# Kernel optimization log

Measured on AMD Instinct MI355X. Metric: run time of the kernel, lower is better.

The kernel has to match this reference:

```python
import jax, jax.numpy as jnp
import numpy as np

N_NODES = 100000
N_EDGES = 3200000
IN_C, HID_C, OUT_C = 128, 16, 5
NEG_SLOPE = 0.2


def setup_inputs() -> dict:
    key = jax.random.key(0)
    ks = jax.random.split(key, 12)
    x = jax.random.normal(ks[0], (N_NODES, IN_C), dtype=jnp.float32)
    edge_index = jax.random.randint(ks[1], (2, N_EDGES), 0, N_NODES, dtype=jnp.int64)
    # GATConv layer 1 params (heads=1)
    s1 = 1.0 / np.sqrt(IN_C)
    W1 = jax.random.uniform(ks[2], (IN_C, HID_C), jnp.float32, -s1, s1)
    att_src1 = jax.random.uniform(ks[3], (HID_C,), jnp.float32, -1.0, 1.0) * s1
    att_dst1 = jax.random.uniform(ks[4], (HID_C,), jnp.float32, -1.0, 1.0) * s1
    b1 = jnp.zeros((HID_C,), jnp.float32)
    # GATConv layer 2 params
    s2 = 1.0 / np.sqrt(HID_C)
    W2 = jax.random.uniform(ks[5], (HID_C, OUT_C), jnp.float32, -s2, s2)
    att_src2 = jax.random.uniform(ks[6], (OUT_C,), jnp.float32, -1.0, 1.0) * s2
    att_dst2 = jax.random.uniform(ks[7], (OUT_C,), jnp.float32, -1.0, 1.0) * s2
    b2 = jnp.zeros((OUT_C,), jnp.float32)
    return {"x": x, "edge_index": edge_index,
            "W1": W1, "att_src1": att_src1, "att_dst1": att_dst1, "b1": b1,
            "W2": W2, "att_src2": att_src2, "att_dst2": att_dst2, "b2": b2}


def gat_layer(x, src, dst, W, att_src, att_dst, bias, n_nodes):
    # project: [N, C_out]
    h = x @ W
    a_src = h @ att_src  # [N]
    a_dst = h @ att_dst  # [N]
    e = a_src[src] + a_dst[dst]            # [E]
    e = jax.nn.leaky_relu(e, NEG_SLOPE)
    # per-destination-node softmax over incoming edges (stable)
    m = jax.ops.segment_max(e, dst, num_segments=n_nodes)
    ex = jnp.exp(e - m[dst])
    denom = jax.ops.segment_sum(ex, dst, num_segments=n_nodes)
    alpha = ex / (denom[dst] + 1e-16)      # [E]
    # weighted scatter-aggregate of source features
    out = jax.ops.segment_sum(h[src] * alpha[:, None], dst, num_segments=n_nodes)
    return out + bias


def reference(x, edge_index, W1, att_src1, att_dst1, b1, W2, att_src2, att_dst2, b2):
    n = x.shape[0]
    loops = jnp.arange(n, dtype=edge_index.dtype)
    src = jnp.concatenate([edge_index[0], loops])  # add_self_loops=True
    dst = jnp.concatenate([edge_index[1], loops])
    h = gat_layer(x, src, dst, W1, att_src1, att_dst1, b1, n)
    h = jax.nn.relu(h)
    h = gat_layer(h, src, dst, W2, att_src2, att_dst2, b2, n)
    return jax.nn.log_softmax(h, axis=1)
```

## Files before the change

### kernel.cpp

```cpp
#include <hip/hip_runtime.h>

#define N_NODES 100000
#define N_EDGES 3200000
#define E_TOT   (N_EDGES + N_NODES)
#define IN_C 128
#define HID  16
#define OUTC 5
#define NEG_SLOPE 0.2f

#define NBKT 391
#define CAP  9216
#define P1_TILE 8192
#define P1_GRID ((E_TOT + P1_TILE - 1) / P1_TILE)

__global__ void zero_gcnt_k(int* __restrict__ gcnt) {
    int i = blockIdx.x * blockDim.x + threadIdx.x;
    if (i < NBKT) gcnt[i] = 0;
}

__global__ __launch_bounds__(256) void part_k(const int* __restrict__ ei,
                                              int* __restrict__ gcnt,
                                              unsigned* __restrict__ pairs) {
    __shared__ unsigned vbuf[P1_TILE];
    __shared__ unsigned short bbuf[P1_TILE];
    __shared__ int hist[NBKT];
    __shared__ int cur[NBKT];
    int t = threadIdx.x;
    for (int i = t; i < NBKT; i += 256) hist[i] = 0;
    __syncthreads();
    int base = blockIdx.x * P1_TILE;
    int lim = E_TOT - base; if (lim > P1_TILE) lim = P1_TILE;
    for (int i = t; i < lim; i += 256) {
        int e = base + i;
        int s, d;
        if (e < N_EDGES) { s = ei[e]; d = ei[N_EDGES + e]; }
        else             { s = e - N_EDGES; d = s; }
        int b = d >> 8;
        vbuf[i] = ((unsigned)s << 8) | (unsigned)(d & 255);
        bbuf[i] = (unsigned short)b;
        atomicAdd(&hist[b], 1);
    }
    __syncthreads();
    for (int i = t; i < NBKT; i += 256) {
        int h = hist[i];
        cur[i] = h ? atomicAdd(&gcnt[i], h) : 0;
    }
    __syncthreads();
    for (int i = t; i < lim; i += 256) {
        int b = bbuf[i];
        int p = atomicAdd(&cur[b], 1);
        if (p >= 0 && p < CAP) pairs[(size_t)b * CAP + p] = vbuf[i];
    }
}

__global__ void scan_gcnt_k(const int* __restrict__ gcnt, int* __restrict__ cbase) {
    __shared__ int s[512];
    int t = threadIdx.x;
    int v = (t < NBKT) ? gcnt[t] : 0;
    s[t] = v; __syncthreads();
    for (int off = 1; off < 512; off <<= 1) {
        int x = (t >= off) ? s[t - off] : 0;
        __syncthreads();
        s[t] += x;
        __syncthreads();
    }
    if (t < NBKT) cbase[t] = s[t] - v;
}

__global__ __launch_bounds__(256) void build_k(const unsigned* __restrict__ pairs,
                                               const int* __restrict__ gcnt,
                                               const int* __restrict__ cbase,
                                               int* __restrict__ csr,
                                               int* __restrict__ row_start,
                                               int* __restrict__ cnt) {
    __shared__ int c[256], s[256], cur[256];
    int t = threadIdx.x;
    int b = blockIdx.x;
    c[t] = 0;
    __syncthreads();
    int tot = gcnt[b];
    if (tot > CAP) tot = CAP;
    size_t pbase = (size_t)b * CAP;
    for (int i = t; i < tot; i += 256) atomicAdd(&c[pairs[pbase + i] & 255u], 1);
    __syncthreads();
    int v0 = c[t];
    s[t] = v0; __syncthreads();
    for (int off = 1; off < 256; off <<= 1) {
        int x = (t >= off) ? s[t - off] : 0;
        __syncthreads();
        s[t] += x;
        __syncthreads();
    }
    int excl = s[t] - v0;
    int gbase = cbase[b];
    int node = (b << 8) + t;
    if (node < N_NODES) { row_start[node] = gbase + excl; cnt[node] = v0; }
    cur[t] = gbase + excl;
    __syncthreads();
    for (int i = t; i < tot; i += 256) {
        unsigned v = pairs[pbase + i];
        int pos = atomicAdd(&cur[v & 255u], 1);
        csr[pos] = (int)(v >> 8);
    }
}

__global__ void proj1_k(const float* __restrict__ x, const float* __restrict__ W1,
                        const float* __restrict__ att_s, const float* __restrict__ att_d,
                        float* __restrict__ h1, float* __restrict__ a_src,
                        float* __restrict__ a_dst) {
    __shared__ float sW[IN_C * HID];
    __shared__ float sX[16 * IN_C];
    __shared__ float sH[16 * HID];
    int t = threadIdx.x;
    for (int i = t; i < IN_C * HID; i += 256) sW[i] = W1[i];
    int node0 = blockIdx.x * 16;
    for (int i = t; i < 16 * IN_C; i += 256) {
        int r = i >> 7, c = i & 127;
        int node = node0 + r;
        sX[i] = (node < N_NODES) ? x[(size_t)node * IN_C + c] : 0.0f;
    }
    __syncthreads();
    int r = t >> 4, c = t & 15;
    int node = node0 + r;
    float acc = 0.0f;
    #pragma unroll 8
    for (int k = 0; k < IN_C; ++k) acc += sX[r * IN_C + k] * sW[k * HID + c];
    sH[r * HID + c] = acc;
    if (node < N_NODES) h1[(size_t)node * HID + c] = acc;
    __syncthreads();
    if (c == 0 && node < N_NODES) {
        float s = 0.0f, d = 0.0f;
        #pragma unroll
        for (int k = 0; k < HID; ++k) {
            float hv = sH[r * HID + k];
            s += hv * att_s[k];
            d += hv * att_d[k];
        }
        a_src[node] = s;
        a_dst[node] = d;
    }
}

#define H2_STRIDE 8
__global__ __launch_bounds__(256) void gat1_k(
    const int* __restrict__ csr, const int* __restrict__ row_start,
    const int* __restrict__ cnt, const float* __restrict__ h1,
    const float* __restrict__ a_src1, const float* __restrict__ a_dst1,
    const float* __restrict__ b1, const float* __restrict__ W2,
    const float* __restrict__ as2, const float* __restrict__ ad2,
    float* __restrict__ h2p, float* __restrict__ a_dst2) {
    __shared__ float sW2[HID * OUTC];
    __shared__ float sB1[HID];
    __shared__ float sAs[OUTC], sAd[OUTC];
    int t = threadIdx.x;
    if (t < HID * OUTC) sW2[t] = W2[t];
    if (t < HID) sB1[t] = b1[t];
    if (t < OUTC) { sAs[t] = as2[t]; sAd[t] = ad2[t]; }
    __syncthreads();

    int node = (blockIdx.x * 256 + t) >> 4;
    int lane = t & 15;
    int start = row_start[node];
    int len   = cnt[node];
    float ad  = a_dst1[node];

    float acc[HID];
    #pragma unroll
    for (int c = 0; c < HID; ++c) acc[c] = 0.0f;
    float accd = 0.0f;
    for (int it = lane; it < len; it += 16) {
        int s = csr[start + it];
        float v = a_src1[s] + ad;
        v = (v > 0.0f) ? v : NEG_SLOPE * v;
        float ex = __expf(v);
        accd += ex;
        const float4* h4 = (const float4*)(h1 + (size_t)s * HID);
        #pragma unroll
        for (int q = 0; q < 4; ++q) {
            float4 hv = h4[q];
            acc[q * 4 + 0] += ex * hv.x;
            acc[q * 4 + 1] += ex * hv.y;
            acc[q * 4 + 2] += ex * hv.z;
            acc[q * 4 + 3] += ex * hv.w;
        }
    }
    #pragma unroll
    for (int off = 8; off; off >>= 1) {
        accd += __shfl_xor(accd, off);
        #pragma unroll
        for (int c = 0; c < HID; ++c) acc[c] += __shfl_xor(acc[c], off);
    }
    float inv = 1.0f / (accd + 1e-16f);
    float g[HID];
    #pragma unroll
    for (int k = 0; k < HID; ++k) g[k] = fmaxf(acc[k] * inv + sB1[k], 0.0f);
    float h2[OUTC];
    #pragma unroll
    for (int c = 0; c < OUTC; ++c) {
        float a = 0.0f;
        #pragma unroll
        for (int k = 0; k < HID; ++k) a += g[k] * sW2[k * OUTC + c];
        h2[c] = a;
    }
    if (lane == 0) {
        float s2 = 0.0f, d2 = 0.0f;
        #pragma unroll
        for (int c = 0; c < OUTC; ++c) { s2 += h2[c] * sAs[c]; d2 += h2[c] * sAd[c]; }
        h2p[(size_t)node * H2_STRIDE] = s2;
        a_dst2[node] = d2;
    }
    if (lane >= 1 && lane <= OUTC) {
        float hv = 0.0f;
        #pragma unroll
        for (int c = 0; c < OUTC; ++c) if (lane - 1 == c) hv = h2[c];
        h2p[(size_t)node * H2_STRIDE + lane] = hv;
    }
}

__global__ __launch_bounds__(256) void gat2_k(
    const int* __restrict__ csr, const int* __restrict__ row_start,
    const int* __restrict__ cnt, const float* __restrict__ h2p,
    const float* __restrict__ a_dst2, const float* __restrict__ b2,
    float* __restrict__ out) {
    __shared__ float sB2[OUTC];
    int t = threadIdx.x;
    if (t < OUTC) sB2[t] = b2[t];
    __syncthreads();

    int node = (blockIdx.x * 256 + t) >> 4;
    int lane = t & 15;
    int start = row_start[node];
    int len   = cnt[node];
    float ad  = a_dst2[node];

    float acc[OUTC];
    #pragma unroll
    for (int c = 0; c < OUTC; ++c) acc[c] = 0.0f;
    float accd = 0.0f;
    for (int it = lane; it < len; it += 16) {
        int s = csr[start + it];
        const float4* hp = (const float4*)(h2p + (size_t)s * H2_STRIDE);
        float4 p0 = hp[0];
        float4 p1 = hp[1];
        float v = p0.x + ad;
        v = (v > 0.0f) ? v : NEG_SLOPE * v;
        float ex = __expf(v);
        accd += ex;
        acc[0] += ex * p0.y; acc[1] += ex * p0.z; acc[2] += ex * p0.w;
        acc[3] += ex * p1.x; acc[4] += ex * p1.y;
    }
    #pragma unroll
    for (int off = 8; off; off >>= 1) {
        accd += __shfl_xor(accd, off);
        #pragma unroll
        for (int c = 0; c < OUTC; ++c) acc[c] += __shfl_xor(acc[c], off);
    }
    float inv = 1.0f / (accd + 1e-16f);
    float val[OUTC];
    float mx = -3.4e38f;
    #pragma unroll
    for (int c = 0; c < OUTC; ++c) {
        val[c] = acc[c] * inv + sB2[c];
        mx = fmaxf(mx, val[c]);
    }
    float se = 0.0f;
    #pragma unroll
    for (int c = 0; c < OUTC; ++c) se += __expf(val[c] - mx);
    float lse = logf(se) + mx;
    if (lane < OUTC) {
        float v = 0.0f;
        #pragma unroll
        for (int c = 0; c < OUTC; ++c) if (lane == c) v = val[c];
        out[(size_t)node * OUTC + lane] = v - lse;
    }
}

extern "C" void kernel_launch(void* const* d_in, const int* in_sizes, int n_in,
                              void* d_out, int out_size, void* d_ws, size_t ws_size,
                              hipStream_t stream) {
    const float* x    = (const float*)d_in[0];
    const int*   ei   = (const int*)d_in[1];
    const float* W1   = (const float*)d_in[2];
    const float* as1  = (const float*)d_in[3];
    const float* ad1  = (const float*)d_in[4];
    const float* b1   = (const float*)d_in[5];
    const float* W2   = (const float*)d_in[6];
    const float* as2  = (const float*)d_in[7];
    const float* ad2  = (const float*)d_in[8];
    const float* b2   = (const float*)d_in[9];
    float* out = (float*)d_out;

    int* wsi = (int*)d_ws;
    unsigned* pairs  = (unsigned*)wsi;
    float* h1    = (float*)wsi;
    float* h2p   = h1 + (size_t)16 * N_NODES;
    float* asrc1 = h1 + (size_t)24 * N_NODES;
    float* adst1 = h1 + (size_t)25 * N_NODES;
    float* adst2 = h1 + (size_t)26 * N_NODES;
    int* csr       = wsi + (size_t)NBKT * CAP;
    int* cnt       = csr + E_TOT;
    int* row_start = cnt + N_NODES;
    int* gcnt      = row_start + N_NODES;
    int* cbase     = gcnt + NBKT;

    const int B = 256;
    const int gW = (N_NODES * 16) / B;

    zero_gcnt_k<<<(NBKT + B - 1) / B, B, 0, stream>>>(gcnt);
    part_k<<<P1_GRID, B, 0, stream>>>(ei, gcnt, pairs);
    scan_gcnt_k<<<1, 512, 0, stream>>>(gcnt, cbase);
    build_k<<<NBKT, B, 0, stream>>>(pairs, gcnt, cbase, csr, row_start, cnt);

    proj1_k<<<(N_NODES + 15) / 16, 256, 0, stream>>>(x, W1, as1, ad1, h1, asrc1, adst1);
    gat1_k<<<gW, B, 0, stream>>>(csr, row_start, cnt, h1, asrc1, adst1, b1,
                                 W2, as2, ad2, h2p, adst2);
    gat2_k<<<gW, B, 0, stream>>>(csr, row_start, cnt, h2p, adst2, b2, out);
}
```

Baseline: 286.7 us.

## Aggregate directly from bucketed edge pairs with LDS atomics; drop CSR build; fp16 features

Removes the scan and CSR build kernels. The two GAT aggregation kernels now read the per-bucket edge pairs directly, with each 512-thread block handling half of a 256-node bucket and accumulating weighted features into shared memory through atomics. Node features h1 and h2 are stored as fp16 to cut gather bandwidth. The cost is heavy shared-memory atomic contention, each pair being read twice with half the threads skipping, and reduced precision in the features.

```diff
diff --git a/kernel.cpp b/kernel.cpp
--- a/kernel.cpp
+++ b/kernel.cpp
@@ -1,4 +1,5 @@
 #include <hip/hip_runtime.h>
+#include <hip/hip_fp16.h>
 
 #define N_NODES 100000
 #define N_EDGES 3200000
@@ -12,6 +13,14 @@
 #define CAP  9216
 #define P1_TILE 8192
 #define P1_GRID ((E_TOT + P1_TILE - 1) / P1_TILE)
+
+__device__ __forceinline__ float pk_half2(float a, float b) {
+    __half2 h = __halves2half2(__float2half(a), __float2half(b));
+    return *(float*)&h;
+}
+__device__ __forceinline__ float2 unpk_half2(float v) {
+    return __half22float2(*(__half2*)&v);
+}
 
 __global__ void zero_gcnt_k(int* __restrict__ gcnt) {
     int i = blockIdx.x * blockDim.x + threadIdx.x;
@@ -53,60 +62,9 @@
     }
 }
 
-__global__ void scan_gcnt_k(const int* __restrict__ gcnt, int* __restrict__ cbase) {
-    __shared__ int s[512];
-    int t = threadIdx.x;
-    int v = (t < NBKT) ? gcnt[t] : 0;
-    s[t] = v; __syncthreads();
-    for (int off = 1; off < 512; off <<= 1) {
-        int x = (t >= off) ? s[t - off] : 0;
-        __syncthreads();
-        s[t] += x;
-        __syncthreads();
-    }
-    if (t < NBKT) cbase[t] = s[t] - v;
-}
-
-__global__ __launch_bounds__(256) void build_k(const unsigned* __restrict__ pairs,
-                                               const int* __restrict__ gcnt,
-                                               const int* __restrict__ cbase,
-                                               int* __restrict__ csr,
-                                               int* __restrict__ row_start,
-                                               int* __restrict__ cnt) {
-    __shared__ int c[256], s[256], cur[256];
-    int t = threadIdx.x;
-    int b = blockIdx.x;
-    c[t] = 0;
-    __syncthreads();
-    int tot = gcnt[b];
-    if (tot > CAP) tot = CAP;
-    size_t pbase = (size_t)b * CAP;
-    for (int i = t; i < tot; i += 256) atomicAdd(&c[pairs[pbase + i] & 255u], 1);
-    __syncthreads();
-    int v0 = c[t];
-    s[t] = v0; __syncthreads();
-    for (int off = 1; off < 256; off <<= 1) {
-        int x = (t >= off) ? s[t - off] : 0;
-        __syncthreads();
-        s[t] += x;
-        __syncthreads();
-    }
-    int excl = s[t] - v0;
-    int gbase = cbase[b];
-    int node = (b << 8) + t;
-    if (node < N_NODES) { row_start[node] = gbase + excl; cnt[node] = v0; }
-    cur[t] = gbase + excl;
-    __syncthreads();
-    for (int i = t; i < tot; i += 256) {
-        unsigned v = pairs[pbase + i];
-        int pos = atomicAdd(&cur[v & 255u], 1);
-        csr[pos] = (int)(v >> 8);
-    }
-}
-
 __global__ void proj1_k(const float* __restrict__ x, const float* __restrict__ W1,
                         const float* __restrict__ att_s, const float* __restrict__ att_d,
-                        float* __restrict__ h1, float* __restrict__ a_src,
+                        __half* __restrict__ h1f, float* __restrict__ a_src,
                         float* __restrict__ a_dst) {
     __shared__ float sW[IN_C * HID];
     __shared__ float sX[16 * IN_C];
@@ -126,7 +84,7 @@
     #pragma unroll 8
     for (int k = 0; k < IN_C; ++k) acc += sX[r * IN_C + k] * sW[k * HID + c];
     sH[r * HID + c] = acc;
-    if (node < N_NODES) h1[(size_t)node * HID + c] = acc;
+    if (node < N_NODES) h1f[(size_t)node * HID + c] = __float2half(acc);
     __syncthreads();
     if (c == 0 && node < N_NODES) {
         float s = 0.0f, d = 0.0f;
@@ -141,137 +99,144 @@
     }
 }
 
-#define H2_STRIDE 8
-__global__ __launch_bounds__(256) void gat1_k(
-    const int* __restrict__ csr, const int* __restrict__ row_start,
-    const int* __restrict__ cnt, const float* __restrict__ h1,
-    const float* __restrict__ a_src1, const float* __restrict__ a_dst1,
-    const float* __restrict__ b1, const float* __restrict__ W2,
-    const float* __restrict__ as2, const float* __restrict__ ad2,
-    float* __restrict__ h2p, float* __restrict__ a_dst2) {
+__global__ __launch_bounds__(512) void gat1b_k(
+    const unsigned* __restrict__ pairs, const int* __restrict__ gcnt,
+    const __half* __restrict__ h1f, const float* __restrict__ asrc1,
+    const float* __restrict__ adst1, const float* __restrict__ b1,
+    const float* __restrict__ W2, const float* __restrict__ as2,
+    const float* __restrict__ ad2, float4* __restrict__ h2p,
+    float* __restrict__ adst2) {
+    __shared__ float acc[128][17];
+    __shared__ float adt[128];
     __shared__ float sW2[HID * OUTC];
     __shared__ float sB1[HID];
     __shared__ float sAs[OUTC], sAd[OUTC];
     int t = threadIdx.x;
+    int bk = blockIdx.x >> 1, hh = blockIdx.x & 1;
+    for (int i = t; i < 128 * 17; i += 512) ((float*)acc)[i] = 0.0f;
     if (t < HID * OUTC) sW2[t] = W2[t];
-    if (t < HID) sB1[t] = b1[t];
-    if (t < OUTC) { sAs[t] = as2[t]; sAd[t] = ad2[t]; }
-    __syncthreads();
-
-    int node = (blockIdx.x * 256 + t) >> 4;
-    int lane = t & 15;
-    int start = row_start[node];
-    int len   = cnt[node];
-    float ad  = a_dst1[node];
-
-    float acc[HID];
-    #pragma unroll
-    for (int c = 0; c < HID; ++c) acc[c] = 0.0f;
-    float accd = 0.0f;
-    for (int it = lane; it < len; it += 16) {
-        int s = csr[start + it];
-        float v = a_src1[s] + ad;
-        v = (v > 0.0f) ? v : NEG_SLOPE * v;
-        float ex = __expf(v);
-        accd += ex;
-        const float4* h4 = (const float4*)(h1 + (size_t)s * HID);
-        #pragma unroll
-        for (int q = 0; q < 4; ++q) {
-            float4 hv = h4[q];
-            acc[q * 4 + 0] += ex * hv.x;
-            acc[q * 4 + 1] += ex * hv.y;
-            acc[q * 4 + 2] += ex * hv.z;
-            acc[q * 4 + 3] += ex * hv.w;
+    else if (t >= 96 && t < 96 + HID) sB1[t - 96] = b1[t - 96];
+    else if (t >= 128 && t < 128 + OUTC) sAs[t - 128] = as2[t - 128];
+    else if (t >= 160 && t < 160 + OUTC) sAd[t - 160] = ad2[t - 160];
+    if (t >= 256 && t < 384) {
+        int node = (bk << 8) + (hh << 7) + (t - 256);
+        adt[t - 256] = (node < N_NODES) ? adst1[node] : 0.0f;
+    }
+    __syncthreads();
+    int tot = gcnt[bk]; if (tot > CAP) tot = CAP;
+    size_t pb = (size_t)bk * CAP;
+    for (int i = t; i < tot; i += 512) {
+        unsigned v = pairs[pb + i];
+        int dl8 = (int)(v & 255u);
+        if ((dl8 >> 7) != hh) continue;
+        int dl = dl8 & 127;
+        int s = (int)(v >> 8);
+        float e = asrc1[s] + adt[dl];
+        e = (e > 0.0f) ? e : NEG_SLOPE * e;
+        float ex = __expf(e);
+        const float4* hp = (const float4*)(h1f + (size_t)s * HID);
+        float4 r0 = hp[0], r1 = hp[1];
+        float2 f0 = unpk_half2(r0.x), f1 = unpk_half2(r0.y);
+        float2 f2 = unpk_half2(r0.z), f3 = unpk_half2(r0.w);
+        float2 f4 = unpk_half2(r1.x), f5 = unpk_half2(r1.y);
+        float2 f6 = unpk_half2(r1.z), f7 = unpk_half2(r1.w);
+        atomicAdd(&acc[dl][0],  ex * f0.x); atomicAdd(&acc[dl][1],  ex * f0.y);
+        atomicAdd(&acc[dl][2],  ex * f1.x); atomicAdd(&acc[dl][3],  ex * f1.y);
+        atomicAdd(&acc[dl][4],  ex * f2.x); atomicAdd(&acc[dl][5],  ex * f2.y);
+        atomicAdd(&acc[dl][6],  ex * f3.x); atomicAdd(&acc[dl][7],  ex * f3.y);
+        atomicAdd(&acc[dl][8],  ex * f4.x); atomicAdd(&acc[dl][9],  ex * f4.y);
+        atomicAdd(&acc[dl][10], ex * f5.x); atomicAdd(&acc[dl][11], ex * f5.y);
+        atomicAdd(&acc[dl][12], ex * f6.x); atomicAdd(&acc[dl][13], ex * f6.y);
+        atomicAdd(&acc[dl][14], ex * f7.x); atomicAdd(&acc[dl][15], ex * f7.y);
+        atomicAdd(&acc[dl][16], ex);
+    }
+    __syncthreads();
+    if (t < 128) {
+        int node = (bk << 8) + (hh << 7) + t;
+        if (node < N_NODES) {
+            float inv = 1.0f / (acc[t][16] + 1e-16f);
+            float g[HID];
+            #pragma unroll
+            for (int k = 0; k < HID; ++k)
+                g[k] = fmaxf(acc[t][k] * inv + sB1[k], 0.0f);
+            float h2[OUTC];
+            #pragma unroll
+            for (int c = 0; c < OUTC; ++c) {
+                float a = 0.0f;
+                #pragma unroll
+                for (int k = 0; k < HID; ++k) a += g[k] * sW2[k * OUTC + c];
+                h2[c] = a;
+            }
+            float s2 = 0.0f, d2 = 0.0f;
+            #pragma unroll
+            for (int c = 0; c < OUTC; ++c) { s2 += h2[c] * sAs[c]; d2 += h2[c] * sAd[c]; }
+            adst2[node] = d2;
+            float4 r;
+            r.x = s2;
+            r.y = pk_half2(h2[0], h2[1]);
+            r.z = pk_half2(h2[2], h2[3]);
+            r.w = pk_half2(h2[4], 0.0f);
+            h2p[node] = r;
         }
     }
-    #pragma unroll
-    for (int off = 8; off; off >>= 1) {
-        accd += __shfl_xor(accd, off);
-        #pragma unroll
-        for (int c = 0; c < HID; ++c) acc[c] += __shfl_xor(acc[c], off);
-    }
-    float inv = 1.0f / (accd + 1e-16f);
-    float g[HID];
-    #pragma unroll
-    for (int k = 0; k < HID; ++k) g[k] = fmaxf(acc[k] * inv + sB1[k], 0.0f);
-    float h2[OUTC];
-    #pragma unroll
-    for (int c = 0; c < OUTC; ++c) {
-        float a = 0.0f;
-        #pragma unroll
-        for (int k = 0; k < HID; ++k) a += g[k] * sW2[k * OUTC + c];
-        h2[c] = a;
-    }
-    if (lane == 0) {
-        float s2 = 0.0f, d2 = 0.0f;
-        #pragma unroll
-        for (int c = 0; c < OUTC; ++c) { s2 += h2[c] * sAs[c]; d2 += h2[c] * sAd[c]; }
-        h2p[(size_t)node * H2_STRIDE] = s2;
-        a_dst2[node] = d2;
-    }
-    if (lane >= 1 && lane <= OUTC) {
-        float hv = 0.0f;
-        #pragma unroll
-        for (int c = 0; c < OUTC; ++c) if (lane - 1 == c) hv = h2[c];
-        h2p[(size_t)node * H2_STRIDE + lane] = hv;
-    }
-}
-
-__global__ __launch_bounds__(256) void gat2_k(
-    const int* __restrict__ csr, const int* __restrict__ row_start,
-    const int* __restrict__ cnt, const float* __restrict__ h2p,
-    const float* __restrict__ a_dst2, const float* __restrict__ b2,
-    float* __restrict__ out) {
+}
+
+__global__ __launch_bounds__(512) void gat2b_k(
+    const unsigned* __restrict__ pairs, const int* __restrict__ gcnt,
+    const float4* __restrict__ h2p, const float* __restrict__ adst2,
+    const float* __restrict__ b2, float* __restrict__ out) {
+    __shared__ float acc[128][7];
+    __shared__ float adt[128];
     __shared__ float sB2[OUTC];
     int t = threadIdx.x;
+    int bk = blockIdx.x >> 1, hh = blockIdx.x & 1;
+    for (int i = t; i < 128 * 7; i += 512) ((float*)acc)[i] = 0.0f;
     if (t < OUTC) sB2[t] = b2[t];
-    __syncthreads();
-
-    int node = (blockIdx.x * 256 + t) >> 4;
-    int lane = t & 15;
-    int start = row_start[node];
-    int len   = cnt[node];
-    float ad  = a_dst2[node];
-
-    float acc[OUTC];
-    #pragma unroll
-    for (int c = 0; c < OUTC; ++c) acc[c] = 0.0f;
-    float accd = 0.0f;
-    for (int it = lane; it < len; it += 16) {
-        int s = csr[start + it];
-        const float4* hp = (const float4*)(h2p + (size_t)s * H2_STRIDE);
-        float4 p0 = hp[0];
-        float4 p1 = hp[1];
-        float v = p0.x + ad;
-        v = (v > 0.0f) ? v : NEG_SLOPE * v;
-        float ex = __expf(v);
-        accd += ex;
-        acc[0] += ex * p0.y; acc[1] += ex * p0.z; acc[2] += ex * p0.w;
-        acc[3] += ex * p1.x; acc[4] += ex * p1.y;
-    }
-    #pragma unroll
-    for (int off = 8; off; off >>= 1) {
-        accd += __shfl_xor(accd, off);
-        #pragma unroll
-        for (int c = 0; c < OUTC; ++c) acc[c] += __shfl_xor(acc[c], off);
-    }
-    float inv = 1.0f / (accd + 1e-16f);
-    float val[OUTC];
-    float mx = -3.4e38f;
-    #pragma unroll
-    for (int c = 0; c < OUTC; ++c) {
-        val[c] = acc[c] * inv + sB2[c];
-        mx = fmaxf(mx, val[c]);
-    }
-    float se = 0.0f;
-    #pragma unroll
-    for (int c = 0; c < OUTC; ++c) se += __expf(val[c] - mx);
-    float lse = logf(se) + mx;
-    if (lane < OUTC) {
-        float v = 0.0f;
-        #pragma unroll
-        for (int c = 0; c < OUTC; ++c) if (lane == c) v = val[c];
-        out[(size_t)node * OUTC + lane] = v - lse;
+    if (t >= 64 && t < 192) {
+        int node = (bk << 8) + (hh << 7) + (t - 64);
+        adt[t - 64] = (node < N_NODES) ? adst2[node] : 0.0f;
+    }
+    __syncthreads();
+    int tot = gcnt[bk]; if (tot > CAP) tot = CAP;
+    size_t pb = (size_t)bk * CAP;
+    for (int i = t; i < tot; i += 512) {
+        unsigned v = pairs[pb + i];
+        int dl8 = (int)(v & 255u);
+        if ((dl8 >> 7) != hh) continue;
+        int dl = dl8 & 127;
+        int s = (int)(v >> 8);
+        float4 r = h2p[s];
+        float e = r.x + adt[dl];
+        e = (e > 0.0f) ? e : NEG_SLOPE * e;
+        float ex = __expf(e);
+        float2 f01 = unpk_half2(r.y);
+        float2 f23 = unpk_half2(r.z);
+        float2 f4_ = unpk_half2(r.w);
+        atomicAdd(&acc[dl][0], ex * f01.x); atomicAdd(&acc[dl][1], ex * f01.y);
+        atomicAdd(&acc[dl][2], ex * f23.x); atomicAdd(&acc[dl][3], ex * f23.y);
+        atomicAdd(&acc[dl][4], ex * f4_.x);
+        atomicAdd(&acc[dl][5], ex);
+    }
+    __syncthreads();
+    if (t < 128) {
+        int node = (bk << 8) + (hh << 7) + t;
+        if (node < N_NODES) {
+            float inv = 1.0f / (acc[t][5] + 1e-16f);
+            float val[OUTC];
+            float mx = -3.4e38f;
+            #pragma unroll
+            for (int c = 0; c < OUTC; ++c) {
+                val[c] = acc[t][c] * inv + sB2[c];
+                mx = fmaxf(mx, val[c]);
+            }
+            float se = 0.0f;
+            #pragma unroll
+            for (int c = 0; c < OUTC; ++c) se += __expf(val[c] - mx);
+            float lse = logf(se) + mx;
+            #pragma unroll
+            for (int c = 0; c < OUTC; ++c)
+                out[(size_t)node * OUTC + c] = val[c] - lse;
+        }
     }
 }
 
@@ -290,29 +255,23 @@
     const float* b2   = (const float*)d_in[9];
     float* out = (float*)d_out;
 
-    int* wsi = (int*)d_ws;
-    unsigned* pairs  = (unsigned*)wsi;
-    float* h1    = (float*)wsi;
-    float* h2p   = h1 + (size_t)16 * N_NODES;
-    float* asrc1 = h1 + (size_t)24 * N_NODES;
-    float* adst1 = h1 + (size_t)25 * N_NODES;
-    float* adst2 = h1 + (size_t)26 * N_NODES;
-    int* csr       = wsi + (size_t)NBKT * CAP;
-    int* cnt       = csr + E_TOT;
-    int* row_start = cnt + N_NODES;
-    int* gcnt      = row_start + N_NODES;
-    int* cbase     = gcnt + NBKT;
+    char* wsb = (char*)d_ws;
+    unsigned* pairs = (unsigned*)wsb;
+    float4* h2p     = (float4*)(wsb + (size_t)NBKT * CAP * 4);
+    __half* h1f     = (__half*)((char*)h2p + (size_t)N_NODES * 16);
+    float* asrc1    = (float*)((char*)h1f + (size_t)N_NODES * HID * 2);
+    float* adst1    = asrc1 + N_NODES;
+    float* adst2    = adst1 + N_NODES;
+    int*   gcnt     = (int*)(adst2 + N_NODES);
 
     const int B = 256;
-    const int gW = (N_NODES * 16) / B;
+    const int gB = NBKT * 2;
 
     zero_gcnt_k<<<(NBKT + B - 1) / B, B, 0, stream>>>(gcnt);
     part_k<<<P1_GRID, B, 0, stream>>>(ei, gcnt, pairs);
-    scan_gcnt_k<<<1, 512, 0, stream>>>(gcnt, cbase);
-    build_k<<<NBKT, B, 0, stream>>>(pairs, gcnt, cbase, csr, row_start, cnt);
-
-    proj1_k<<<(N_NODES + 15) / 16, 256, 0, stream>>>(x, W1, as1, ad1, h1, asrc1, adst1);
-    gat1_k<<<gW, B, 0, stream>>>(csr, row_start, cnt, h1, asrc1, adst1, b1,
-                                 W2, as2, ad2, h2p, adst2);
-    gat2_k<<<gW, B, 0, stream>>>(csr, row_start, cnt, h2p, adst2, b2, out);
-}
+
+    proj1_k<<<(N_NODES + 15) / 16, 256, 0, stream>>>(x, W1, as1, ad1, h1f, asrc1, adst1);
+    gat1b_k<<<gB, 512, 0, stream>>>(pairs, gcnt, h1f, asrc1, adst1, b1,
+                                    W2, as2, ad2, h2p, adst2);
+    gat2b_k<<<gB, 512, 0, stream>>>(pairs, gcnt, h2p, adst2, b2, out);
+}
```

Result: slower. 675.9 us (+135.7%).
